# Kernel tuning notes

Hardware: AMD Instinct MI355X
Metric: run time of the kernel (lower is better)

## Reference

```python
import jax, jax.numpy as jnp
import numpy as np

NEG_SLOPE = 0.2  # PyG GATv2Conv default leaky_relu slope


def _gatv2(x, src, dst, eattr, Wl, bl, Wr, br, We, att, bias, N):
    """GATv2Conv (concat heads, eval mode -> no dropout).
    x: [N, Fin], src/dst: [E], eattr: [E, Fe], att: [H, C]."""
    H, C = att.shape
    xl = (x @ Wl.T + bl).reshape(N, H, C)   # lin_l -> source features
    xr = (x @ Wr.T + br).reshape(N, H, C)   # lin_r -> target features
    ea = (eattr @ We.T).reshape(-1, H, C)   # lin_edge (no bias)
    m = xl[src] + xr[dst] + ea              # [E, H, C]
    m = jnp.where(m >= 0, m, NEG_SLOPE * m)
    logits = jnp.einsum('ehc,hc->eh', m, att)  # [E, H]
    # segment softmax over incoming edges of each target node
    lmax = jax.ops.segment_max(logits, dst, num_segments=N)  # self-loops -> nonempty
    ex = jnp.exp(logits - lmax[dst])
    denom = jax.ops.segment_sum(ex, dst, num_segments=N)
    alpha = ex / denom[dst]                 # [E, H]
    out = jax.ops.segment_sum(alpha[:, :, None] * xl[src], dst, num_segments=N)
    return out.reshape(N, H * C) + bias


def setup_inputs() -> dict:
    key = jax.random.key(0)
    ks = jax.random.split(key, 24)
    B, num_nodes, Fn, Fe, deg = 16, 5000, 64, 16, 32
    N = B * num_nodes
    E = N * deg
    s = 0.05
    inp = {
        'x': jax.random.normal(ks[0], (N, Fn), jnp.float32),
        'edge_index': jax.random.randint(ks[1], (2, E), 0, N, jnp.int64),
        'edge_attr': jax.random.normal(ks[2], (E, Fe), jnp.float32),
        'num_nodes': num_nodes,
        'W1l': jax.random.normal(ks[3], (9, Fn), jnp.float32) * s,
        'b1l': jnp.zeros((9,), jnp.float32),
        'W1r': jax.random.normal(ks[4], (9, Fn), jnp.float32) * s,
        'b1r': jnp.zeros((9,), jnp.float32),
        'We1': jax.random.normal(ks[5], (9, Fe), jnp.float32) * s,
        'att1': jax.random.normal(ks[6], (3, 3), jnp.float32) * s,
        'bias1': jnp.zeros((9,), jnp.float32),
        'W2l': jax.random.normal(ks[7], (20, 9), jnp.float32) * s,
        'b2l': jnp.zeros((20,), jnp.float32),
        'W2r': jax.random.normal(ks[8], (20, 9), jnp.float32) * s,
        'b2r': jnp.zeros((20,), jnp.float32),
        'We2': jax.random.normal(ks[9], (20, Fe), jnp.float32) * s,
        'att2': jax.random.normal(ks[10], (4, 5), jnp.float32) * s,
        'bias2': jnp.zeros((20,), jnp.float32),
        'fcW1': jax.random.normal(ks[11], (100, 20 * num_nodes), jnp.float32) * 0.01,
        'fcb1': jnp.zeros((100,), jnp.float32),
        'fcW2': jax.random.normal(ks[12], (10, 100), jnp.float32) * s,
        'fcb2': jnp.zeros((10,), jnp.float32),
        'fcW3': jax.random.normal(ks[13], (1, 10), jnp.float32) * s,
        'fcb3': jnp.zeros((1,), jnp.float32),
    }
    return inp


def reference(x, edge_index, edge_attr, num_nodes,
              W1l, b1l, W1r, b1r, We1, att1, bias1,
              W2l, b2l, W2r, b2r, We2, att2, bias2,
              fcW1, fcb1, fcW2, fcb2, fcW3, fcb3):
    N = x.shape[0]
    src0, dst0 = edge_index[0], edge_index[1]
    # add_self_loops=True, fill_value='mean': loop attr = mean of incoming edge attrs
    cnt = jax.ops.segment_sum(jnp.ones((src0.shape[0],), x.dtype), dst0, num_segments=N)
    loop_attr = jax.ops.segment_sum(edge_attr, dst0, num_segments=N) / jnp.maximum(cnt, 1.0)[:, None]
    nodes = jnp.arange(N)
    src = jnp.concatenate([src0, nodes])
    dst = jnp.concatenate([dst0, nodes])
    ea = jnp.concatenate([edge_attr, loop_attr], axis=0)

    h = _gatv2(x, src, dst, ea, W1l, b1l, W1r, b1r, We1, att1, bias1, N)
    h = jax.nn.relu(h)
    h = _gatv2(h, src, dst, ea, W2l, b2l, W2r, b2r, We2, att2, bias2, N)
    h = jax.nn.relu(h)

    B = N // num_nodes
    h = h.reshape(B, num_nodes * 20)
    h = jax.nn.relu(h @ fcW1.T + fcb1)
    h = jax.nn.relu(h @ fcW2.T + fcb2)
    return h @ fcW3.T + fcb3
```

## Files before the change

### kernel.cpp

```cpp
#include <hip/hip_runtime.h>
#include <math.h>

#define TPB   256
#define NPB   256
#define MAXNB 512
#define BCAP  10240
#define ITEMS 16
#define CPAD  16

static inline int gridFor(size_t n) { return (int)((n + TPB - 1) / TPB); }


__global__ void __launch_bounds__(TPB) k_lin1(
    const float* __restrict__ x,
    const float* __restrict__ Wl, const float* __restrict__ bl,
    const float* __restrict__ Wr, const float* __restrict__ br,
    float* __restrict__ xl, float* __restrict__ xr, int N)
{
  int idx = blockIdx.x * TPB + threadIdx.x;
  if (idx >= N * 18) return;
  int i = idx / 18, t = idx % 18;
  bool left = t < 9;
  int j = left ? t : t - 9;
  const float4* W4 = (const float4*)((left ? Wl : Wr) + j * 64);
  float s = (left ? bl : br)[j];
  const float4* xi4 = (const float4*)(x + (size_t)i * 64);
#pragma unroll
  for (int f = 0; f < 16; f++) {
    float4 xv = xi4[f], wv = W4[f];
    s = fmaf(xv.x, wv.x, s);
    s = fmaf(xv.y, wv.y, s);
    s = fmaf(xv.z, wv.z, s);
    s = fmaf(xv.w, wv.w, s);
  }
  (left ? xl : xr)[(size_t)i * 9 + j] = s;
}

__global__ void __launch_bounds__(TPB) k_lin2(
    const float* __restrict__ h1, const float* __restrict__ bias1,
    const float* __restrict__ Wl, const float* __restrict__ bl,
    const float* __restrict__ Wr, const float* __restrict__ br,
    float* __restrict__ xl, float* __restrict__ xr, int N)
{
  int idx = blockIdx.x * TPB + threadIdx.x;
  if (idx >= N * 40) return;
  int i = idx / 40, t = idx % 40;
  float hr[9];
#pragma unroll
  for (int k = 0; k < 9; k++) hr[k] = fmaxf(h1[(size_t)i * 9 + k] + bias1[k], 0.0f);
  bool left = t < 20;
  int j = left ? t : t - 20;
  const float* W = (left ? Wl : Wr) + j * 9;
  float s = (left ? bl : br)[j];
#pragma unroll
  for (int k = 0; k < 9; k++) s = fmaf(hr[k], W[k], s);
  (left ? xl : xr)[(size_t)i * 20 + j] = s;
}


__global__ void __launch_bounds__(TPB) k_bin(
    const int* __restrict__ ei, int* __restrict__ bucketCntP,
    int2* __restrict__ staging, int E, int NB)
{
  __shared__ int hist[MAXNB];
  __shared__ int base[MAXNB];
  int tid = threadIdx.x;
  size_t tile0 = (size_t)blockIdx.x * (TPB * ITEMS);
  for (int i = tid; i < NB; i += TPB) hist[i] = 0;
  __syncthreads();
  for (int it = 0; it < ITEMS; ++it) {
    size_t e = tile0 + (size_t)it * TPB + tid;
    if (e < (size_t)E) {
      int dst = ei[(size_t)E + e];
      atomicAdd(&hist[dst >> 8], 1);
    }
  }
  __syncthreads();
  for (int i = tid; i < NB; i += TPB) {
    int c = hist[i];
    base[i] = c ? atomicAdd(&bucketCntP[(size_t)i * CPAD], c) : 0;
    hist[i] = 0;
  }
  __syncthreads();
  for (int it = 0; it < ITEMS; ++it) {
    size_t e = tile0 + (size_t)it * TPB + tid;
    if (e < (size_t)E) {
      int src = ei[e];
      int dst = ei[(size_t)E + e];
      int b = dst >> 8;
      int r = atomicAdd(&hist[b], 1);
      staging[(size_t)b * BCAP + base[b] + r] =
          make_int2((int)e | ((dst & 255) << 22), src);
    }
  }
}


__global__ void __launch_bounds__(MAXNB) k_scanb(
    const int* __restrict__ bucketCntP, int* __restrict__ bucketBase, int NB)
{
  __shared__ int s[MAXNB];
  int tid = threadIdx.x;
  int v = (tid < NB) ? bucketCntP[(size_t)tid * CPAD] : 0;
  s[tid] = v;
  __syncthreads();
  for (int off = 1; off < MAXNB; off <<= 1) {
    int u = (tid >= off) ? s[tid - off] : 0;
    __syncthreads();
    s[tid] += u;
    __syncthreads();
  }
  if (tid < NB) bucketBase[tid] = s[tid] - v;
}


__global__ void __launch_bounds__(TPB) k_csr(
    const int2* __restrict__ staging, const int* __restrict__ bucketCntP,
    const int* __restrict__ bucketBase,
    int* __restrict__ rowptr, int* __restrict__ degO,
    int* __restrict__ src_csr, int* __restrict__ eid_csr, int N)
{
  int b = blockIdx.x, tid = threadIdx.x;
  int n0 = b << 8;
  int recCnt = bucketCntP[(size_t)b * CPAD];
  int ebase = bucketBase[b];
  const int2* rec = staging + (size_t)b * BCAP;
  __shared__ int deg_s[NPB];
  __shared__ int pfx[NPB];
  __shared__ int cur[NPB];
  deg_s[tid] = 0;
  __syncthreads();
  for (int r = tid; r < recCnt; r += TPB)
    atomicAdd(&deg_s[(rec[r].x >> 22) & 255], 1);
  __syncthreads();
  pfx[tid] = deg_s[tid];
  __syncthreads();
  for (int off = 1; off < NPB; off <<= 1) {
    int u = (tid >= off) ? pfx[tid - off] : 0;
    __syncthreads();
    pfx[tid] += u;
    __syncthreads();
  }
  int excl = pfx[tid] - deg_s[tid];
  int n = n0 + tid;
  if (n < N) { rowptr[n] = ebase + excl; degO[n] = deg_s[tid]; }
  cur[tid] = ebase + excl;
  __syncthreads();
  for (int r = tid; r < recCnt; r += TPB) {
    int2 rc = rec[r];
    int dl = (rc.x >> 22) & 255;
    int eid = rc.x & 0x3FFFFF;
    int pos = atomicAdd(&cur[dl], 1);
    src_csr[pos] = rc.y;
    eid_csr[pos] = eid;
  }
}


template <int H, int C, int L>
__global__ void __launch_bounds__(TPB) k_attn(
    const int* __restrict__ rowptr, const int* __restrict__ deg,
    const int* __restrict__ src_csr, const int* __restrict__ eid_csr,
    const float* __restrict__ eattr,
    const float* __restrict__ xl, const float* __restrict__ xr,
    const float* __restrict__ We, const float* __restrict__ att,
    const float* __restrict__ bias,
    float* __restrict__ out, int N)
{
  constexpr int HC = H * C;
  int idx = blockIdx.x * TPB + threadIdx.x;
  if (idx >= N * H * L) return;
  int l = idx & (L - 1);
  int g = idx / L;
  int n = g / H, h = g - n * H;

  float w[C][16];
#pragma unroll
  for (int c = 0; c < C; c++)
#pragma unroll
    for (int f = 0; f < 16; f++) w[c][f] = We[(h * C + c) * 16 + f];
  float attv[C], xrv[C];
#pragma unroll
  for (int c = 0; c < C; c++) {
    attv[c] = att[h * C + c];
    xrv[c] = xr[(size_t)n * HC + h * C + c];
  }

  int r0 = rowptr[n];
  int dg = deg[n];

  float mx = -3.0e38f, den = 0.0f;
  float acc[C], ea_sum[C];
#pragma unroll
  for (int c = 0; c < C; c++) { acc[c] = 0.0f; ea_sum[c] = 0.0f; }

  int p = l;
  int ecur = 0, scur = 0;
  if (p < dg) { ecur = eid_csr[r0 + p]; scur = src_csr[r0 + p]; }
  while (p < dg) {
    int pn = p + L;
    int enx = 0, snx = 0;
    if (pn < dg) { enx = eid_csr[r0 + pn]; snx = src_csr[r0 + pn]; }

    float a[16];
    const float4* a4 = (const float4*)(eattr + (size_t)ecur * 16);
#pragma unroll
    for (int k = 0; k < 4; k++) {
      float4 v = a4[k];
      a[4 * k + 0] = v.x; a[4 * k + 1] = v.y; a[4 * k + 2] = v.z; a[4 * k + 3] = v.w;
    }
    const float* xs = xl + (size_t)scur * HC + h * C;
    float xv[C];
#pragma unroll
    for (int c = 0; c < C; c++) xv[c] = xs[c];
    float lg = 0.0f;
#pragma unroll
    for (int c = 0; c < C; c++) {
      float ea = 0.0f;
#pragma unroll
      for (int f = 0; f < 16; f++) ea = fmaf(a[f], w[c][f], ea);
      ea_sum[c] += ea;
      float m = xv[c] + xrv[c] + ea;
      m = (m >= 0.0f) ? m : 0.2f * m;
      lg = fmaf(m, attv[c], lg);
    }
    float nm = fmaxf(mx, lg);
    float s = expf(mx - nm);
    float wE = expf(lg - nm);
    den = den * s + wE;
#pragma unroll
    for (int c = 0; c < C; c++) acc[c] = fmaf(acc[c], s, wE * xv[c]);
    mx = nm;

    p = pn; ecur = enx; scur = snx;
  }

#pragma unroll
  for (int off = 1; off < L; off <<= 1) {
    float omx  = __shfl_xor(mx, off, 64);
    float oden = __shfl_xor(den, off, 64);
    float nm = fmaxf(mx, omx);
    float s1 = expf(mx - nm);
    float s2 = expf(omx - nm);
    den = den * s1 + oden * s2;
#pragma unroll
    for (int c = 0; c < C; c++) {
      float oa = __shfl_xor(acc[c], off, 64);
      float oe = __shfl_xor(ea_sum[c], off, 64);
      acc[c] = acc[c] * s1 + oa * s2;
      ea_sum[c] += oe;
    }
    mx = nm;
  }

  {
    float invd = 1.0f / fmaxf((float)dg, 1.0f);
    const float* xs = xl + (size_t)n * HC + h * C;
    float xv[C];
#pragma unroll
    for (int c = 0; c < C; c++) xv[c] = xs[c];
    float lg = 0.0f;
#pragma unroll
    for (int c = 0; c < C; c++) {
      float m = xv[c] + xrv[c] + ea_sum[c] * invd;
      m = (m >= 0.0f) ? m : 0.2f * m;
      lg = fmaf(m, attv[c], lg);
    }
    float nm = fmaxf(mx, lg);
    float s = expf(mx - nm);
    float wE = expf(lg - nm);
    den = den * s + wE;
#pragma unroll
    for (int c = 0; c < C; c++) acc[c] = fmaf(acc[c], s, wE * xv[c]);
  }

  float inv = 1.0f / den;
  float* od = out + (size_t)n * HC + h * C;
  for (int c = l; c < C; c += L) {
    float v = acc[c] * inv;
    if (bias) v = fmaxf(v + bias[h * C + c], 0.0f);
    od[c] = v;
  }
}


__global__ void __launch_bounds__(TPB) k_fc1(
    const float* __restrict__ h2, const float* __restrict__ W,
    float* __restrict__ h3, int NN, int Kc)
{
  int o = blockIdx.x;
  int ks = blockIdx.y;
  int k0 = ks * Kc;
  int k1 = min(NN, k0 + Kc);
  float acc[16];
#pragma unroll
  for (int b = 0; b < 16; b++) acc[b] = 0.0f;
  const float* wo = W + (size_t)o * NN;
  for (int k = k0 + threadIdx.x; k < k1; k += TPB) {
    float w = wo[k];
#pragma unroll
    for (int b = 0; b < 16; b++) acc[b] = fmaf(h2[(size_t)b * NN + k], w, acc[b]);
  }
#pragma unroll
  for (int b = 0; b < 16; b++) {
    float v = acc[b];
#pragma unroll
    for (int off = 32; off > 0; off >>= 1) v += __shfl_down(v, off, 64);
    if ((threadIdx.x & 63) == 0) atomicAdd(&h3[b * 100 + o], v);
  }
}

__global__ void __launch_bounds__(TPB) k_fc23(
    const float* __restrict__ h3, const float* __restrict__ fcb1,
    const float* __restrict__ W2, const float* __restrict__ b2,
    const float* __restrict__ W3, const float* __restrict__ b3,
    float* __restrict__ out, int B)
{
  __shared__ float s3[32 * 100];
  __shared__ float s4[32 * 10];
  int tid = threadIdx.x;
  for (int t = tid; t < B * 100; t += TPB)
    s3[t] = fmaxf(h3[t] + fcb1[t % 100], 0.0f);
  __syncthreads();
  if (tid < B * 10) {
    int b = tid / 10, o = tid % 10;
    float s = b2[o];
#pragma unroll
    for (int k = 0; k < 100; k++) s = fmaf(s3[b * 100 + k], W2[o * 100 + k], s);
    s4[tid] = fmaxf(s, 0.0f);
  }
  __syncthreads();
  if (tid < B) {
    float s = b3[0];
#pragma unroll
    for (int k = 0; k < 10; k++) s = fmaf(s4[tid * 10 + k], W3[k], s);
    out[tid] = s;
  }
}


extern "C" void kernel_launch(void* const* d_in, const int* in_sizes, int n_in,
                              void* d_out, int out_size, void* d_ws, size_t ws_size,
                              hipStream_t stream) {
  const float* x      = (const float*)d_in[0];
  const int*   ei     = (const int*)d_in[1];
  const float* eattr  = (const float*)d_in[2];
  const float* W1l = (const float*)d_in[4];  const float* b1l = (const float*)d_in[5];
  const float* W1r = (const float*)d_in[6];  const float* b1r = (const float*)d_in[7];
  const float* We1 = (const float*)d_in[8];  const float* att1 = (const float*)d_in[9];
  const float* bias1 = (const float*)d_in[10];
  const float* W2l = (const float*)d_in[11]; const float* b2l = (const float*)d_in[12];
  const float* W2r = (const float*)d_in[13]; const float* b2r = (const float*)d_in[14];
  const float* We2 = (const float*)d_in[15]; const float* att2 = (const float*)d_in[16];
  const float* bias2 = (const float*)d_in[17];
  const float* fcW1 = (const float*)d_in[18]; const float* fcb1 = (const float*)d_in[19];
  const float* fcW2 = (const float*)d_in[20]; const float* fcb2 = (const float*)d_in[21];
  const float* fcW3 = (const float*)d_in[22]; const float* fcb3 = (const float*)d_in[23];
  float* out = (float*)d_out;

  const int N = in_sizes[0] / 64;
  const int E = in_sizes[2] / 16;
  const int num_nodes = in_sizes[18] / (100 * 20);
  const int B = N / num_nodes;
  const int NB = (N + NPB - 1) / NPB;

  char* base = (char*)d_ws;
  size_t off = 0;
  auto alloc = [&](size_t bytes) {
    size_t o = off; off += (bytes + 63) & ~(size_t)63; return o;
  };
  size_t o_bcnt   = alloc((size_t)NB * CPAD * 4);
  size_t o_h3     = alloc((size_t)B * 100 * 4);
  size_t zeroBytes = off;
  size_t o_bbase  = alloc((size_t)NB * 4);
  size_t o_stage  = alloc((size_t)NB * BCAP * 8);
  size_t o_rowptr = alloc((size_t)N * 4);
  size_t o_deg    = alloc((size_t)N * 4);
  size_t o_srcc   = alloc((size_t)E * 4);
  size_t o_eidc   = alloc((size_t)E * 4);
  size_t o_xl1    = alloc((size_t)N * 9 * 4);
  size_t o_xr1    = alloc((size_t)N * 9 * 4);
  size_t o_xl2    = alloc((size_t)N * 20 * 4);
  size_t o_xr2    = alloc((size_t)N * 20 * 4);
  size_t o_h1     = alloc((size_t)N * 9 * 4);
  size_t o_h2     = alloc((size_t)N * 20 * 4);

  int*   bcnt   = (int*)(base + o_bcnt);
  float* h3     = (float*)(base + o_h3);
  int*   bbase  = (int*)(base + o_bbase);
  int2*  stage  = (int2*)(base + o_stage);
  int*   rowptr = (int*)(base + o_rowptr);
  int*   deg    = (int*)(base + o_deg);
  int*   srcc   = (int*)(base + o_srcc);
  int*   eidc   = (int*)(base + o_eidc);
  float* xl1    = (float*)(base + o_xl1);
  float* xr1    = (float*)(base + o_xr1);
  float* xl2    = (float*)(base + o_xl2);
  float* xr2    = (float*)(base + o_xr2);
  float* h1     = (float*)(base + o_h1);
  float* h2     = (float*)(base + o_h2);

  hipMemsetAsync(d_ws, 0, zeroBytes, stream);

  k_lin1<<<gridFor((size_t)N * 18), TPB, 0, stream>>>(x, W1l, b1l, W1r, b1r, xl1, xr1, N);

  int binBlocks = (int)(((size_t)E + TPB * ITEMS - 1) / (TPB * ITEMS));
  k_bin<<<binBlocks, TPB, 0, stream>>>(ei, bcnt, stage, E, NB);
  k_scanb<<<1, MAXNB, 0, stream>>>(bcnt, bbase, NB);
  k_csr<<<NB, TPB, 0, stream>>>(stage, bcnt, bbase, rowptr, deg, srcc, eidc, N);

  k_attn<3, 3, 8><<<gridFor((size_t)N * 3 * 8), TPB, 0, stream>>>(
      rowptr, deg, srcc, eidc, eattr, xl1, xr1, We1, att1, nullptr, h1, N);

  k_lin2<<<gridFor((size_t)N * 40), TPB, 0, stream>>>(h1, bias1, W2l, b2l, W2r, b2r, xl2, xr2, N);

  k_attn<4, 5, 8><<<gridFor((size_t)N * 4 * 8), TPB, 0, stream>>>(
      rowptr, deg, srcc, eidc, eattr, xl2, xr2, We2, att2, bias2, h2, N);

  const int NN = num_nodes * 20;
  const int KS = 16;
  const int Kc = (NN + KS - 1) / KS;
  dim3 g1(100, KS);
  k_fc1<<<g1, TPB, 0, stream>>>(h2, fcW1, h3, NN, Kc);
  k_fc23<<<1, TPB, 0, stream>>>(h3, fcb1, fcW2, fcb2, fcW3, fcb3, out, B);
  (void)out_size; (void)n_in;
}
```

Baseline: 745.0 us.

## Pad per-head features for float4 loads, pack CSR edges, deepen prefetch

Pads the xl/xr node features so each head starts on a 16-byte boundary (4 floats per head in layer 1, 8 in layer 2), which lets the attention kernel fetch them with float4 loads. The CSR src and edge-id arrays are merged into one int2 array so each edge needs a single load. The attention loop now prefetches the next edge's attributes and source features one iteration ahead, and the edge index two ahead. Lanes per (node, head) drop from 8 to 4, giving each thread more edges to process. This costs extra memory footprint and register pressure from the padding and the prefetch buffers.

Result: no change. 740.2 us (-0.6%).

```diff
diff --git a/kernel.cpp b/kernel.cpp
--- a/kernel.cpp
+++ b/kernel.cpp
@@ -33,7 +33,8 @@
     s = fmaf(xv.z, wv.z, s);
     s = fmaf(xv.w, wv.w, s);
   }
-  (left ? xl : xr)[(size_t)i * 9 + j] = s;
+  int h = j / 3, c = j - h * 3;
+  (left ? xl : xr)[(size_t)i * 12 + h * 4 + c] = s;
 }
 
 __global__ void __launch_bounds__(TPB) k_lin2(
@@ -54,7 +55,8 @@
   float s = (left ? bl : br)[j];
 #pragma unroll
   for (int k = 0; k < 9; k++) s = fmaf(hr[k], W[k], s);
-  (left ? xl : xr)[(size_t)i * 20 + j] = s;
+  int h = j / 5, c = j - h * 5;
+  (left ? xl : xr)[(size_t)i * 32 + h * 8 + c] = s;
 }
 
 
@@ -118,7 +120,7 @@
     const int2* __restrict__ staging, const int* __restrict__ bucketCntP,
     const int* __restrict__ bucketBase,
     int* __restrict__ rowptr, int* __restrict__ degO,
-    int* __restrict__ src_csr, int* __restrict__ eid_csr, int N)
+    int2* __restrict__ es, int N)
 {
   int b = blockIdx.x, tid = threadIdx.x;
   int n0 = b << 8;
@@ -151,18 +153,17 @@
     int dl = (rc.x >> 22) & 255;
     int eid = rc.x & 0x3FFFFF;
     int pos = atomicAdd(&cur[dl], 1);
-    src_csr[pos] = rc.y;
-    eid_csr[pos] = eid;
-  }
-}
-
-
-template <int H, int C, int L>
+    es[pos] = make_int2(rc.y, eid);
+  }
+}
+
+
+template <int H, int C, int L, int CP>
 __global__ void __launch_bounds__(TPB) k_attn(
     const int* __restrict__ rowptr, const int* __restrict__ deg,
-    const int* __restrict__ src_csr, const int* __restrict__ eid_csr,
+    const int2* __restrict__ es,
     const float* __restrict__ eattr,
-    const float* __restrict__ xl, const float* __restrict__ xr,
+    const float* __restrict__ xlp, const float* __restrict__ xrp,
     const float* __restrict__ We, const float* __restrict__ att,
     const float* __restrict__ bias,
     float* __restrict__ out, int N)
@@ -179,11 +180,22 @@
   for (int c = 0; c < C; c++)
 #pragma unroll
     for (int f = 0; f < 16; f++) w[c][f] = We[(h * C + c) * 16 + f];
-  float attv[C], xrv[C];
-#pragma unroll
-  for (int c = 0; c < C; c++) {
-    attv[c] = att[h * C + c];
-    xrv[c] = xr[(size_t)n * HC + h * C + c];
+  float attv[C];
+#pragma unroll
+  for (int c = 0; c < C; c++) attv[c] = att[h * C + c];
+
+  float xrv[C];
+  {
+    const float4* r4 = (const float4*)(xrp + ((size_t)n * H + h) * CP);
+    float4 R0 = r4[0];
+    float rf[8];
+    rf[0] = R0.x; rf[1] = R0.y; rf[2] = R0.z; rf[3] = R0.w;
+    if constexpr (CP == 8) {
+      float4 R1 = r4[1];
+      rf[4] = R1.x; rf[5] = R1.y; rf[6] = R1.z; rf[7] = R1.w;
+    }
+#pragma unroll
+    for (int c = 0; c < C; c++) xrv[c] = rf[c];
   }
 
   int r0 = rowptr[n];
@@ -195,24 +207,45 @@
   for (int c = 0; c < C; c++) { acc[c] = 0.0f; ea_sum[c] = 0.0f; }
 
   int p = l;
-  int ecur = 0, scur = 0;
-  if (p < dg) { ecur = eid_csr[r0 + p]; scur = src_csr[r0 + p]; }
+  int2 e0 = make_int2(0, 0), e1 = make_int2(0, 0);
+  if (p < dg)     e0 = es[r0 + p];
+  if (p + L < dg) e1 = es[r0 + p + L];
+  float4 A0, A1, A2, A3, X0, X1;
+  if (p < dg) {
+    const float4* a4 = (const float4*)(eattr + (size_t)e0.y * 16);
+    A0 = a4[0]; A1 = a4[1]; A2 = a4[2]; A3 = a4[3];
+    const float4* x4 = (const float4*)(xlp + ((size_t)e0.x * H + h) * CP);
+    X0 = x4[0];
+    if constexpr (CP == 8) X1 = x4[1];
+  }
+
   while (p < dg) {
     int pn = p + L;
-    int enx = 0, snx = 0;
-    if (pn < dg) { enx = eid_csr[r0 + pn]; snx = src_csr[r0 + pn]; }
+    float4 B0, B1, B2, B3, Y0, Y1;
+    if (pn < dg) {
+      const float4* a4 = (const float4*)(eattr + (size_t)e1.y * 16);
+      B0 = a4[0]; B1 = a4[1]; B2 = a4[2]; B3 = a4[3];
+      const float4* x4 = (const float4*)(xlp + ((size_t)e1.x * H + h) * CP);
+      Y0 = x4[0];
+      if constexpr (CP == 8) Y1 = x4[1];
+    }
+    int2 e2 = make_int2(0, 0);
+    if (pn + L < dg) e2 = es[r0 + pn + L];
 
     float a[16];
-    const float4* a4 = (const float4*)(eattr + (size_t)ecur * 16);
-#pragma unroll
-    for (int k = 0; k < 4; k++) {
-      float4 v = a4[k];
-      a[4 * k + 0] = v.x; a[4 * k + 1] = v.y; a[4 * k + 2] = v.z; a[4 * k + 3] = v.w;
-    }
-    const float* xs = xl + (size_t)scur * HC + h * C;
+    a[0] = A0.x; a[1] = A0.y; a[2]  = A0.z; a[3]  = A0.w;
+    a[4] = A1.x; a[5] = A1.y; a[6]  = A1.z; a[7]  = A1.w;
+    a[8] = A2.x; a[9] = A2.y; a[10] = A2.z; a[11] = A2.w;
+    a[12] = A3.x; a[13] = A3.y; a[14] = A3.z; a[15] = A3.w;
+    float xf[8];
+    xf[0] = X0.x; xf[1] = X0.y; xf[2] = X0.z; xf[3] = X0.w;
+    if constexpr (CP == 8) {
+      xf[4] = X1.x; xf[5] = X1.y; xf[6] = X1.z; xf[7] = X1.w;
+    }
     float xv[C];
 #pragma unroll
-    for (int c = 0; c < C; c++) xv[c] = xs[c];
+    for (int c = 0; c < C; c++) xv[c] = xf[c];
+
     float lg = 0.0f;
 #pragma unroll
     for (int c = 0; c < C; c++) {
@@ -232,7 +265,11 @@
     for (int c = 0; c < C; c++) acc[c] = fmaf(acc[c], s, wE * xv[c]);
     mx = nm;
 
-    p = pn; ecur = enx; scur = snx;
+    p = pn;
+    e0 = e1; e1 = e2;
+    A0 = B0; A1 = B1; A2 = B2; A3 = B3;
+    X0 = Y0;
+    if constexpr (CP == 8) X1 = Y1;
   }
 
 #pragma unroll
@@ -255,10 +292,17 @@
 
   {
     float invd = 1.0f / fmaxf((float)dg, 1.0f);
-    const float* xs = xl + (size_t)n * HC + h * C;
+    const float4* x4 = (const float4*)(xlp + ((size_t)n * H + h) * CP);
+    float4 S0 = x4[0];
+    float sf[8];
+    sf[0] = S0.x; sf[1] = S0.y; sf[2] = S0.z; sf[3] = S0.w;
+    if constexpr (CP == 8) {
+      float4 S1 = x4[1];
+      sf[4] = S1.x; sf[5] = S1.y; sf[6] = S1.z; sf[7] = S1.w;
+    }
     float xv[C];
 #pragma unroll
-    for (int c = 0; c < C; c++) xv[c] = xs[c];
+    for (int c = 0; c < C; c++) xv[c] = sf[c];
     float lg = 0.0f;
 #pragma unroll
     for (int c = 0; c < C; c++) {
@@ -376,12 +420,11 @@
   size_t o_stage  = alloc((size_t)NB * BCAP * 8);
   size_t o_rowptr = alloc((size_t)N * 4);
   size_t o_deg    = alloc((size_t)N * 4);
-  size_t o_srcc   = alloc((size_t)E * 4);
-  size_t o_eidc   = alloc((size_t)E * 4);
-  size_t o_xl1    = alloc((size_t)N * 9 * 4);
-  size_t o_xr1    = alloc((size_t)N * 9 * 4);
-  size_t o_xl2    = alloc((size_t)N * 20 * 4);
-  size_t o_xr2    = alloc((size_t)N * 20 * 4);
+  size_t o_es     = alloc((size_t)E * 8);
+  size_t o_xl1    = alloc((size_t)N * 12 * 4);
+  size_t o_xr1    = alloc((size_t)N * 12 * 4);
+  size_t o_xl2    = alloc((size_t)N * 32 * 4);
+  size_t o_xr2    = alloc((size_t)N * 32 * 4);
   size_t o_h1     = alloc((size_t)N * 9 * 4);
   size_t o_h2     = alloc((size_t)N * 20 * 4);
 
@@ -391,8 +434,7 @@
   int2*  stage  = (int2*)(base + o_stage);
   int*   rowptr = (int*)(base + o_rowptr);
   int*   deg    = (int*)(base + o_deg);
-  int*   srcc   = (int*)(base + o_srcc);
-  int*   eidc   = (int*)(base + o_eidc);
+  int2*  es     = (int2*)(base + o_es);
   float* xl1    = (float*)(base + o_xl1);
   float* xr1    = (float*)(base + o_xr1);
   float* xl2    = (float*)(base + o_xl2);
@@ -407,15 +449,15 @@
   int binBlocks = (int)(((size_t)E + TPB * ITEMS - 1) / (TPB * ITEMS));
   k_bin<<<binBlocks, TPB, 0, stream>>>(ei, bcnt, stage, E, NB);
   k_scanb<<<1, MAXNB, 0, stream>>>(bcnt, bbase, NB);
-  k_csr<<<NB, TPB, 0, stream>>>(stage, bcnt, bbase, rowptr, deg, srcc, eidc, N);
-
-  k_attn<3, 3, 8><<<gridFor((size_t)N * 3 * 8), TPB, 0, stream>>>(
-      rowptr, deg, srcc, eidc, eattr, xl1, xr1, We1, att1, nullptr, h1, N);
+  k_csr<<<NB, TPB, 0, stream>>>(stage, bcnt, bbase, rowptr, deg, es, N);
+
+  k_attn<3, 3, 4, 4><<<gridFor((size_t)N * 3 * 4), TPB, 0, stream>>>(
+      rowptr, deg, es, eattr, xl1, xr1, We1, att1, nullptr, h1, N);
 
   k_lin2<<<gridFor((size_t)N * 40), TPB, 0, stream>>>(h1, bias1, W2l, b2l, W2r, b2r, xl2, xr2, N);
 
-  k_attn<4, 5, 8><<<gridFor((size_t)N * 4 * 8), TPB, 0, stream>>>(
-      rowptr, deg, srcc, eidc, eattr, xl2, xr2, We2, att2, bias2, h2, N);
+  k_attn<4, 5, 4, 8><<<gridFor((size_t)N * 4 * 4), TPB, 0, stream>>>(
+      rowptr, deg, es, eattr, xl2, xr2, We2, att2, bias2, h2, N);
 
   const int NN = num_nodes * 20;
   const int KS = 16;
```
